# Kernel tuning notes

Measured on AMD Instinct MI355X. Metric: run time of the kernel, lower is better.

## Reference

```python
import jax, jax.numpy as jnp
import numpy as np

K = 5            # dimW
PARAM_SIGMA = 0.08
LAMBDA_V = 2.0
C_MID = 192


def _conv5(x, w, b):
    # standard 5x5 SAME conv (the linear 'm' term of INRF)
    y = jax.lax.conv_general_dilated(x, w, (1, 1), 'SAME',
                                     dimension_numbers=('NCHW', 'OIHW', 'NCHW'))
    return y + b[None, :, None, None]


def _inrf(x, m_w, m_b, w_w):
    """INRF layer: out = (m * x) - lambda * sum_y w(y) sigma(x(y) - (g*x)(center)).
    dimG=1 so the Gaussian g*x is the identity (center pixel). The radiometric
    nonlinearity sigma is a saturating tanh with slope 1/paramSigma.
    """
    B, C, H, W = x.shape
    # windowed gather: [B, C*K*K, H, W], channel-major / spatial-minor ordering
    patches = jax.lax.conv_general_dilated_patches(x, (K, K), (1, 1), 'SAME')
    patches = patches.reshape(B, C, K * K, H, W)
    s = jnp.tanh((patches - x[:, :, None]) / PARAM_SIGMA)   # [B,C,KK,H,W]
    wterm = jnp.einsum('bckhw,ock->bohw', s, w_w)           # [B,Cout,H,W]
    return _conv5(x, m_w, m_b) - LAMBDA_V * wterm


def _maxpool2(x):
    return jax.lax.reduce_window(x, -jnp.inf, jax.lax.max,
                                 (1, 1, 2, 2), (1, 1, 2, 2), 'VALID')


def _avgpool8(x):
    s = jax.lax.reduce_window(x, 0.0, jax.lax.add,
                              (1, 1, 8, 8), (1, 1, 8, 8), 'VALID')
    return s / 64.0


def setup_inputs() -> dict:
    key = jax.random.key(0)
    ks = jax.random.split(key, 11)
    B = 64
    f32 = jnp.float32
    return {
        'x':    jax.random.normal(ks[0], (B, 3, 32, 32), f32),
        'm1_w': jax.random.normal(ks[1], (C_MID, 3, K, K), f32) * 0.05,
        'm1_b': jnp.zeros((C_MID,), f32),
        'w1_w': jax.random.normal(ks[2], (C_MID, 3, K * K), f32) * 0.05,
        'm2_w': jax.random.normal(ks[3], (C_MID, C_MID, K, K), f32) * 0.02,
        'm2_b': jnp.zeros((C_MID,), f32),
        'w2_w': jax.random.normal(ks[4], (C_MID, C_MID, K * K), f32) * 0.02,
        'm3_w': jax.random.normal(ks[5], (C_MID, C_MID, K, K), f32) * 0.02,
        'm3_b': jnp.zeros((C_MID,), f32),
        'w3_w': jax.random.normal(ks[6], (C_MID, C_MID, K * K), f32) * 0.02,
        'fc_w': jax.random.normal(ks[7], (10, C_MID), f32) * 0.05,
        'fc_b': jnp.zeros((10,), f32),
    }


def reference(x, m1_w, m1_b, w1_w, m2_w, m2_b, w2_w,
              m3_w, m3_b, w3_w, fc_w, fc_b):
    # dropout layers run in eval mode (identity); dp2d1 has p=0.0 anyway
    x00 = _maxpool2(_inrf(x, m1_w, m1_b, w1_w))      # [B,192,16,16]
    x01 = _inrf(x00, m2_w, m2_b, w2_w)               # [B,192,16,16]
    x03 = _maxpool2(x01)                             # [B,192,8,8]
    x04 = _inrf(x03, m3_w, m3_b, w3_w)               # [B,192,8,8]
    x05 = _avgpool8(x04)                             # [B,192,1,1]
    feat = x05.reshape(-1, C_MID)
    logits = feat @ fc_w.T + fc_b                    # [B,10]
    return (logits, x00, x01)
```

## Files before the change

### kernel.cpp

```cpp
#include <hip/hip_runtime.h>
#include <math.h>

#define COUT 192
#define NF 12

typedef __bf16 bf16_8 __attribute__((ext_vector_type(8)));
typedef float  f32x4  __attribute__((ext_vector_type(4)));

__device__ __forceinline__ float fast_tanh125(float d) {
    float e = __builtin_amdgcn_exp2f(d * 36.06737602222409f);
    return 1.0f - 2.0f * __builtin_amdgcn_rcpf(e + 1.0f);
}

__device__ __forceinline__ void gl_lds16(const void* gptr, void* lptr) {
    auto g = (const __attribute__((address_space(1))) unsigned int*)gptr;
    auto l = (__attribute__((address_space(3))) unsigned int*)lptr;
    __builtin_amdgcn_global_load_lds(g, l, 16, 0, 0);
}

template<int CIN>
__global__ void prep_w(const float* __restrict__ m_w, const float* __restrict__ w_w,
                       __bf16* __restrict__ Bp) {
    int idx = blockIdx.x * 256 + threadIdx.x;
    const int total = CIN * 2 * NF * 64;
    if (idx >= total) return;
    int lane = idx & 63;
    int nf = (idx >> 6) % NF;
    int cc = idx / (NF * 64);
    int t = cc & 1, c = cc >> 1;
    int n = nf * 16 + (lane & 15);
    int k0 = (lane >> 4) * 8;
    bf16_8 v;
    #pragma unroll
    for (int e = 0; e < 8; ++e) {
        int k = k0 + e;
        float val = 0.f;
        if (k < 25) {
            val = (t == 0) ? m_w[((size_t)n * CIN + c) * 25 + k]
                           : -2.0f * w_w[((size_t)n * CIN + c) * 25 + k];
        }
        v[e] = (__bf16)val;
    }
    *(bf16_8*)(Bp + (size_t)idx * 8) = v;
}

__global__ __launch_bounds__(256, 3) void inrf1_mfma(
    const float* __restrict__ x, const __bf16* __restrict__ Bp,
    const float* __restrict__ bias, float* __restrict__ x00)
{
    __shared__ float win[3][6][36];
    __shared__ float hp[192][33];

    const int b  = blockIdx.x >> 4;
    const int h0 = (blockIdx.x & 15) * 2;
    const int tid = threadIdx.x;
    const int wv = tid >> 6, lane = tid & 63;
    const int hl = wv >> 1, half = wv & 1;
    const int mcol = lane & 15, q = lane >> 4;
    const int wpos = half * 16 + mcol;

    for (int i = tid; i < 3 * 6 * 36; i += 256) {
        int c = i / 216, r = (i / 36) % 6, cc = i % 36;
        int gr = h0 + r - 2, gc = cc - 2;
        float v = 0.f;
        if (gr >= 0 && gr < 32 && gc >= 0 && gc < 32)
            v = x[((size_t)(b * 3 + c) * 32 + gr) * 32 + gc];
        win[c][r][cc] = v;
    }
    __syncthreads();

    int offs[8];
    #pragma unroll
    for (int e = 0; e < 8; ++e) {
        int k = q * 8 + e;
        int kk = (k < 25) ? k : 0;
        offs[e] = (hl + kk / 5) * 36 + wpos + (kk % 5);
    }
    const int cen_off = (hl + 2) * 36 + wpos + 2;

    f32x4 acc[NF];
    #pragma unroll
    for (int j = 0; j < NF; ++j) acc[j] = (f32x4){0.f, 0.f, 0.f, 0.f};

    const float* winf = &win[0][0][0];
    for (int c = 0; c < 3; ++c) {
        const float* wf = winf + c * 216;
        float cen = wf[cen_off];
        bf16_8 av, as_;
        #pragma unroll
        for (int e = 0; e < 8; ++e) {
            float v = wf[offs[e]];
            av[e] = (__bf16)v;
            as_[e] = (__bf16)fast_tanh125(v - cen);
        }
        const bf16_8* b0 = (const bf16_8*)Bp + ((size_t)(c * 2 + 0) * NF) * 64 + lane;
        const bf16_8* b1 = b0 + NF * 64;
        #pragma unroll
        for (int j = 0; j < NF; ++j)
            acc[j] = __builtin_amdgcn_mfma_f32_16x16x32_bf16(av, b0[j * 64], acc[j], 0, 0, 0);
        #pragma unroll
        for (int j = 0; j < NF; ++j)
            acc[j] = __builtin_amdgcn_mfma_f32_16x16x32_bf16(as_, b1[j * 64], acc[j], 0, 0, 0);
    }

    #pragma unroll
    for (int j = 0; j < NF; ++j) {
        int n = j * 16 + mcol;
        hp[n][hl * 16 + half * 8 + q * 2 + 0] = fmaxf(acc[j][0], acc[j][1]);
        hp[n][hl * 16 + half * 8 + q * 2 + 1] = fmaxf(acc[j][2], acc[j][3]);
    }
    __syncthreads();

    const int hpout = h0 >> 1;
    for (int i = tid; i < 192 * 16; i += 256) {
        int n = i >> 4, wp = i & 15;
        float v = fmaxf(hp[n][wp], hp[n][16 + wp]) + bias[n];
        x00[((size_t)(b * COUT + n) * 16 + hpout) * 16 + wp] = v;
    }
}

__global__ __launch_bounds__(256, 1) void inrf2_mfma(
    const float* __restrict__ xin, const __bf16* __restrict__ Bp,
    float* __restrict__ out0, float* __restrict__ part)
{
    constexpr int CPS = 48;
    __shared__ __align__(16) __bf16 Bs[3][24 * 64 * 8];
    __shared__ float win[3][420];

    const int b  = blockIdx.x >> 2;
    const int ks = blockIdx.x & 3;
    const int c0 = ks * CPS;
    const int tid = threadIdx.x;
    const int wv = tid >> 6, lane = tid & 63;
    const int wp = lane & 15, q = lane >> 4;

    int offs[8];
    #pragma unroll
    for (int e = 0; e < 8; ++e) {
        int k = q * 8 + e;
        int kk = (k < 25) ? k : 0;
        offs[e] = (kk / 5) * 21 + (kk % 5);
    }

    const int j0 = tid, j1 = tid + 256;
    const int r0_ = j0 / 20, c0_ = j0 % 20;
    const int r1_ = j1 / 20, c1_ = j1 % 20;
    const int w0i = r0_ * 21 + c0_;
    const int w1i = r1_ * 21 + c1_;
    const bool in1 = j1 < 400;
    const bool ok0 = (r0_ >= 2 && r0_ < 18 && c0_ >= 2 && c0_ < 18);
    const bool ok1 = in1 && (r1_ >= 2 && r1_ < 18 && c1_ >= 2 && c1_ < 18);
    const float* xb = xin + (size_t)b * COUT * 256;

    f32x4 acc[4][12];
    #pragma unroll
    for (int m = 0; m < 4; ++m)
        #pragma unroll
        for (int j = 0; j < 12; ++j) acc[m][j] = (f32x4){0.f, 0.f, 0.f, 0.f};

#define BUILD_A(SLOT, AV, AS)                                              \
    {                                                                      \
        const float* wc = win[(SLOT)];                                     \
        _Pragma("unroll")                                                  \
        for (int m = 0; m < 4; ++m) {                                      \
            const int base = (wv * 4 + m) * 21 + wp;                       \
            float cen = wc[base + 44];                                     \
            _Pragma("unroll")                                              \
            for (int e = 0; e < 8; ++e) {                                  \
                float v = wc[base + offs[e]];                              \
                (AV)[m][e] = (__bf16)v;                                    \
                (AS)[m][e] = (__bf16)fast_tanh125(v - cen);                \
            }                                                              \
        }                                                                  \
    }

    #pragma unroll
    for (int rr = 0; rr < 2; ++rr) {
        const int c = c0 + rr;
        float v0 = 0.f, v1 = 0.f;
        if (ok0) v0 = xb[(size_t)c * 256 + (r0_ - 2) * 16 + (c0_ - 2)];
        if (ok1) v1 = xb[(size_t)c * 256 + (r1_ - 2) * 16 + (c1_ - 2)];
        const __bf16* gB = Bp + (size_t)c * 2 * NF * 64 * 8 + wv * 3072 + lane * 8;
        #pragma unroll
        for (int i = 0; i < 6; ++i)
            gl_lds16(gB + i * 512, &Bs[rr][wv * 3072 + i * 512]);
        win[rr][w0i] = v0;
        if (in1) win[rr][w1i] = v1;
    }
    __syncthreads();

    bf16_8 av[4], as_[4];
    BUILD_A(0, av, as_);

    #pragma unroll 3
    for (int r = 0; r < CPS; ++r) {
        const int sl_cur = r % 3;
        const int sl_n1  = (r + 1) % 3;
        const int sl_n2  = (r + 2) % 3;
        const bool do2 = (r + 2) < CPS;
        const bool do1 = (r + 1) < CPS;

        float v0 = 0.f, v1 = 0.f;
        if (do2) {
            const int c = c0 + r + 2;
            if (ok0) v0 = xb[(size_t)c * 256 + (r0_ - 2) * 16 + (c0_ - 2)];
            if (ok1) v1 = xb[(size_t)c * 256 + (r1_ - 2) * 16 + (c1_ - 2)];
            const __bf16* gB = Bp + (size_t)c * 2 * NF * 64 * 8 + wv * 3072 + lane * 8;
            #pragma unroll
            for (int i = 0; i < 6; ++i)
                gl_lds16(gB + i * 512, &Bs[sl_n2][wv * 3072 + i * 512]);
        }

        bf16_8 avN[4], asN[4];
        if (do1) BUILD_A(sl_n1, avN, asN);

        const bf16_8* Bf = (const bf16_8*)(Bs[sl_cur]) + lane;
        #pragma unroll
        for (int j = 0; j < 12; ++j) {
            bf16_8 fm = Bf[j * 64];
            bf16_8 fs = Bf[(12 + j) * 64];
            #pragma unroll
            for (int m = 0; m < 4; ++m) {
                acc[m][j] = __builtin_amdgcn_mfma_f32_16x16x32_bf16(av[m],  fm, acc[m][j], 0, 0, 0);
                acc[m][j] = __builtin_amdgcn_mfma_f32_16x16x32_bf16(as_[m], fs, acc[m][j], 0, 0, 0);
            }
        }

        if (do2) {
            win[sl_n2][w0i] = v0;
            if (in1) win[sl_n2][w1i] = v1;
        }

        if (do1) {
            #pragma unroll
            for (int m = 0; m < 4; ++m) { av[m] = avN[m]; as_[m] = asN[m]; }
        }
        __syncthreads();
    }
#undef BUILD_A

    float* outp = (ks == 0) ? out0 : (part + (size_t)(ks - 1) * 3145728);
    #pragma unroll
    for (int j = 0; j < 12; ++j) {
        int n = j * 16 + wp;
        #pragma unroll
        for (int m = 0; m < 4; ++m) {
            int h = wv * 4 + m;
            *(f32x4*)&outp[((size_t)(b * COUT + n)) * 256 + h * 16 + q * 4] = acc[m][j];
        }
    }
}

__global__ __launch_bounds__(512) void finish2(
    float* __restrict__ x01, const float* __restrict__ part,
    const float* __restrict__ bias, __bf16* __restrict__ An)
{
    __shared__ float xbuf[8][256];
    const int b  = blockIdx.x / 24;
    const int cg = blockIdx.x % 24;
    const int tid = threadIdx.x;
    const int wv = tid >> 6, lane = tid & 63;
    const int ch = cg * 8 + wv;

    float* p0 = x01 + ((size_t)b * COUT + ch) * 256;
    const float* pp = part + ((size_t)b * COUT + ch) * 256;
    const float bv = bias[ch];
    #pragma unroll
    for (int i = 0; i < 4; ++i) {
        int idx = lane + 64 * i;
        float s = ((p0[idx] + pp[idx]) + pp[idx + 3145728]) + pp[idx + 2 * 3145728] + bv;
        xbuf[wv][idx] = s;
        p0[idx] = s;
    }
    __syncthreads();

    const int ph = lane >> 3, pw = lane & 7;
    const int i0 = ph * 32 + pw * 2;
    float x8 = fmaxf(fmaxf(xbuf[wv][i0], xbuf[wv][i0 + 1]),
                     fmaxf(xbuf[wv][i0 + 16], xbuf[wv][i0 + 17]));

    float myT = 0.f, myW = 0.f;
    #pragma unroll
    for (int k = 0; k < 25; ++k) {
        const int dy = k / 5 - 2, dx = k % 5 - 2;
        const bool valid = (ph + dy >= 0) && (ph + dy < 8) && (pw + dx >= 0) && (pw + dx < 8);
        float nb = __shfl(x8, (lane + dy * 8 + dx) & 63);
        nb = valid ? nb : 0.f;
        float tS = fast_tanh125(nb - x8);
        float wS = nb;
        #pragma unroll
        for (int off = 1; off < 64; off <<= 1) {
            tS += __shfl_xor(tS, off);
            wS += __shfl_xor(wS, off);
        }
        if (lane == k) { myT = tS; myW = wS; }
    }

    const int mt = b >> 4;
    if (lane < 25) {
        const int k = lane;
        const int la = (k >> 3) * 16 + (b & 15);
        const int e = k & 7;
        const int ccW = ch * 2, ccT = ch * 2 + 1;
        An[((size_t)(ccW * 4 + mt) * 64 + la) * 8 + e] = (__bf16)(myW * 0.015625f);
        An[((size_t)(ccT * 4 + mt) * 64 + la) * 8 + e] = (__bf16)(myT * 0.015625f);
    } else if (lane < 32) {
        const int la = 3 * 16 + (b & 15);
        const int e = lane & 7;
        const int ccW = ch * 2, ccT = ch * 2 + 1;
        An[((size_t)(ccW * 4 + mt) * 64 + la) * 8 + e] = (__bf16)0.f;
        An[((size_t)(ccT * 4 + mt) * 64 + la) * 8 + e] = (__bf16)0.f;
    }
}

__global__ __launch_bounds__(512) void gemm3p(
    const __bf16* __restrict__ An, const __bf16* __restrict__ Bp,
    float* __restrict__ part)
{
    const int ks = blockIdx.x;
    const int tid = threadIdx.x;
    const int wv = tid >> 6, lane = tid & 63;
    const int mt = wv & 3, nh = wv >> 2;

    f32x4 acc[6];
    #pragma unroll
    for (int j = 0; j < 6; ++j) acc[j] = (f32x4){0.f, 0.f, 0.f, 0.f};

    for (int i = 0; i < 4; ++i) {
        const int cc = ks * 4 + i;
        bf16_8 a = *(const bf16_8*)(An + ((size_t)(cc * 4 + mt) * 64 + lane) * 8);
        #pragma unroll
        for (int j = 0; j < 6; ++j) {
            bf16_8 bw = *(const bf16_8*)(Bp + ((size_t)(cc * NF + nh * 6 + j) * 64 + lane) * 8);
            acc[j] = __builtin_amdgcn_mfma_f32_16x16x32_bf16(a, bw, acc[j], 0, 0, 0);
        }
    }
    #pragma unroll
    for (int j = 0; j < 6; ++j) {
        int n = (nh * 6 + j) * 16 + (lane & 15);
        *(f32x4*)(part + ((size_t)ks * COUT + n) * 64 + mt * 16 + (lane >> 4) * 4) = acc[j];
    }
}

__global__ __launch_bounds__(256) void logitsk(
    const float* __restrict__ part, const float* __restrict__ m3_b,
    const float* __restrict__ fc_w, const float* __restrict__ fc_b,
    float* __restrict__ logits)
{
    __shared__ float feat[COUT];
    const int b = blockIdx.x;
    const int t = threadIdx.x;
    if (t < COUT) {
        float s = 0.f;
        for (int ks = 0; ks < 96; ++ks) s += part[((size_t)ks * COUT + t) * 64 + b];
        feat[t] = s + m3_b[t];
    }
    __syncthreads();
    if (t < 10) {
        float s = fc_b[t];
        #pragma unroll 8
        for (int c = 0; c < COUT; ++c) s = fmaf(fc_w[t * COUT + c], feat[c], s);
        logits[(size_t)b * 10 + t] = s;
    }
}

extern "C" void kernel_launch(void* const* d_in, const int* in_sizes, int n_in,
                              void* d_out, int out_size, void* d_ws, size_t ws_size,
                              hipStream_t stream) {
    const float* x    = (const float*)d_in[0];
    const float* m1_w = (const float*)d_in[1];
    const float* m1_b = (const float*)d_in[2];
    const float* w1_w = (const float*)d_in[3];
    const float* m2_w = (const float*)d_in[4];
    const float* m2_b = (const float*)d_in[5];
    const float* w2_w = (const float*)d_in[6];
    const float* m3_w = (const float*)d_in[7];
    const float* m3_b = (const float*)d_in[8];
    const float* w3_w = (const float*)d_in[9];
    const float* fc_w = (const float*)d_in[10];
    const float* fc_b = (const float*)d_in[11];

    float* out = (float*)d_out;
    float* ws  = (float*)d_ws;

    float* logits = out;
    float* x00 = out + 640;
    float* x01 = out + 640 + 3145728;

    __bf16* Bp1  = (__bf16*)(ws);
    __bf16* Bp2  = (__bf16*)(ws + 18432);
    __bf16* Bp3  = (__bf16*)(ws + 1198080);
    __bf16* An   = (__bf16*)(ws + 2377728);
    float*  part2 = ws + 2770944;
    float*  part3 = ws + 2770944;

    prep_w<3>  <<<(3   * 2 * NF * 64 + 255) / 256, 256, 0, stream>>>(m1_w, w1_w, Bp1);
    prep_w<192><<<(192 * 2 * NF * 64 + 255) / 256, 256, 0, stream>>>(m2_w, w2_w, Bp2);
    prep_w<192><<<(192 * 2 * NF * 64 + 255) / 256, 256, 0, stream>>>(m3_w, w3_w, Bp3);

    inrf1_mfma<<<64 * 16, 256, 0, stream>>>(x, Bp1, m1_b, x00);
    inrf2_mfma<<<64 * 4, 256, 0, stream>>>(x00, Bp2, x01, part2);
    finish2<<<64 * 24, 512, 0, stream>>>(x01, part2, m2_b, An);
    gemm3p<<<96, 512, 0, stream>>>(An, Bp3, part3);
    logitsk<<<64, 256, 0, stream>>>(part3, m3_b, fc_w, fc_b, logits);
}
```

Before: 222.5 us.

## Split inrf2 output channels across two wave groups and merge weight-prep launches

The layer-2 INRF MFMA kernel now runs 512 threads per block, with eight waves instead of four. Each group of four waves covers the same 16 rows but only half of the 192 output channels, so accumulators per wave drop from 48 to 24 fragments and more waves are in flight. The A-fragment tanh/bf16 build is now duplicated across the two channel halves. The three weight-prep launches are combined into a single kernel to cut launch overhead.

Result: no change. 223.8 us (+0.6%).

```diff
diff --git a/kernel.cpp b/kernel.cpp
--- a/kernel.cpp
+++ b/kernel.cpp
@@ -18,15 +18,21 @@
     __builtin_amdgcn_global_load_lds(g, l, 16, 0, 0);
 }
 
-template<int CIN>
-__global__ void prep_w(const float* __restrict__ m_w, const float* __restrict__ w_w,
-                       __bf16* __restrict__ Bp) {
+__global__ void prep_all(const float* __restrict__ m1_w, const float* __restrict__ w1_w,
+                         const float* __restrict__ m2_w, const float* __restrict__ w2_w,
+                         const float* __restrict__ m3_w, const float* __restrict__ w3_w,
+                         __bf16* __restrict__ Bp1, __bf16* __restrict__ Bp2,
+                         __bf16* __restrict__ Bp3) {
     int idx = blockIdx.x * 256 + threadIdx.x;
-    const int total = CIN * 2 * NF * 64;
-    if (idx >= total) return;
-    int lane = idx & 63;
-    int nf = (idx >> 6) % NF;
-    int cc = idx / (NF * 64);
+    const int N1 = 3 * 2 * NF * 64, N2 = 192 * 2 * NF * 64;
+    const float *mw, *ww; __bf16* Bp; int CIN, li;
+    if (idx < N1)           { mw = m1_w; ww = w1_w; Bp = Bp1; CIN = 3;   li = idx; }
+    else if (idx < N1 + N2) { mw = m2_w; ww = w2_w; Bp = Bp2; CIN = 192; li = idx - N1; }
+    else if (idx < N1 + 2 * N2) { mw = m3_w; ww = w3_w; Bp = Bp3; CIN = 192; li = idx - N1 - N2; }
+    else return;
+    int lane = li & 63;
+    int nf = (li >> 6) % NF;
+    int cc = li / (NF * 64);
     int t = cc & 1, c = cc >> 1;
     int n = nf * 16 + (lane & 15);
     int k0 = (lane >> 4) * 8;
@@ -36,12 +42,12 @@
         int k = k0 + e;
         float val = 0.f;
         if (k < 25) {
-            val = (t == 0) ? m_w[((size_t)n * CIN + c) * 25 + k]
-                           : -2.0f * w_w[((size_t)n * CIN + c) * 25 + k];
+            val = (t == 0) ? mw[((size_t)n * CIN + c) * 25 + k]
+                           : -2.0f * ww[((size_t)n * CIN + c) * 25 + k];
         }
         v[e] = (__bf16)val;
     }
-    *(bf16_8*)(Bp + (size_t)idx * 8) = v;
+    *(bf16_8*)(Bp + (size_t)li * 8) = v;
 }
 
 __global__ __launch_bounds__(256, 3) void inrf1_mfma(
@@ -119,7 +125,7 @@
     }
 }
 
-__global__ __launch_bounds__(256, 1) void inrf2_mfma(
+__global__ __launch_bounds__(512, 2) void inrf2_mfma(
     const float* __restrict__ xin, const __bf16* __restrict__ Bp,
     float* __restrict__ out0, float* __restrict__ part)
 {
@@ -132,6 +138,7 @@
     const int c0 = ks * CPS;
     const int tid = threadIdx.x;
     const int wv = tid >> 6, lane = tid & 63;
+    const int mg = wv & 3, nh = wv >> 2;
     const int wp = lane & 15, q = lane >> 4;
 
     int offs[8];
@@ -142,28 +149,24 @@
         offs[e] = (kk / 5) * 21 + (kk % 5);
     }
 
-    const int j0 = tid, j1 = tid + 256;
-    const int r0_ = j0 / 20, c0_ = j0 % 20;
-    const int r1_ = j1 / 20, c1_ = j1 % 20;
+    const int r0_ = tid / 20, c0_ = tid % 20;
     const int w0i = r0_ * 21 + c0_;
-    const int w1i = r1_ * 21 + c1_;
-    const bool in1 = j1 < 400;
-    const bool ok0 = (r0_ >= 2 && r0_ < 18 && c0_ >= 2 && c0_ < 18);
-    const bool ok1 = in1 && (r1_ >= 2 && r1_ < 18 && c1_ >= 2 && c1_ < 18);
+    const bool in0 = tid < 400;
+    const bool ok0 = in0 && (r0_ >= 2 && r0_ < 18 && c0_ >= 2 && c0_ < 18);
     const float* xb = xin + (size_t)b * COUT * 256;
 
-    f32x4 acc[4][12];
+    f32x4 acc[4][6];
     #pragma unroll
     for (int m = 0; m < 4; ++m)
         #pragma unroll
-        for (int j = 0; j < 12; ++j) acc[m][j] = (f32x4){0.f, 0.f, 0.f, 0.f};
+        for (int j = 0; j < 6; ++j) acc[m][j] = (f32x4){0.f, 0.f, 0.f, 0.f};
 
 #define BUILD_A(SLOT, AV, AS)                                              \
     {                                                                      \
         const float* wc = win[(SLOT)];                                     \
         _Pragma("unroll")                                                  \
         for (int m = 0; m < 4; ++m) {                                      \
-            const int base = (wv * 4 + m) * 21 + wp;                       \
+            const int base = (mg * 4 + m) * 21 + wp;                       \
             float cen = wc[base + 44];                                     \
             _Pragma("unroll")                                              \
             for (int e = 0; e < 8; ++e) {                                  \
@@ -177,15 +180,13 @@
     #pragma unroll
     for (int rr = 0; rr < 2; ++rr) {
         const int c = c0 + rr;
-        float v0 = 0.f, v1 = 0.f;
+        float v0 = 0.f;
         if (ok0) v0 = xb[(size_t)c * 256 + (r0_ - 2) * 16 + (c0_ - 2)];
-        if (ok1) v1 = xb[(size_t)c * 256 + (r1_ - 2) * 16 + (c1_ - 2)];
-        const __bf16* gB = Bp + (size_t)c * 2 * NF * 64 * 8 + wv * 3072 + lane * 8;
-        #pragma unroll
-        for (int i = 0; i < 6; ++i)
-            gl_lds16(gB + i * 512, &Bs[rr][wv * 3072 + i * 512]);
-        win[rr][w0i] = v0;
-        if (in1) win[rr][w1i] = v1;
+        const __bf16* gB = Bp + (size_t)c * 12288 + wv * 1536 + lane * 8;
+        #pragma unroll
+        for (int i = 0; i < 3; ++i)
+            gl_lds16(gB + i * 512, &Bs[rr][wv * 1536 + i * 512]);
+        if (in0) win[rr][w0i] = v0;
     }
     __syncthreads();
 
@@ -200,15 +201,14 @@
         const bool do2 = (r + 2) < CPS;
         const bool do1 = (r + 1) < CPS;
 
-        float v0 = 0.f, v1 = 0.f;
+        float v0 = 0.f;
         if (do2) {
             const int c = c0 + r + 2;
             if (ok0) v0 = xb[(size_t)c * 256 + (r0_ - 2) * 16 + (c0_ - 2)];
-            if (ok1) v1 = xb[(size_t)c * 256 + (r1_ - 2) * 16 + (c1_ - 2)];
-            const __bf16* gB = Bp + (size_t)c * 2 * NF * 64 * 8 + wv * 3072 + lane * 8;
+            const __bf16* gB = Bp + (size_t)c * 12288 + wv * 1536 + lane * 8;
             #pragma unroll
-            for (int i = 0; i < 6; ++i)
-                gl_lds16(gB + i * 512, &Bs[sl_n2][wv * 3072 + i * 512]);
+            for (int i = 0; i < 3; ++i)
+                gl_lds16(gB + i * 512, &Bs[sl_n2][wv * 1536 + i * 512]);
         }
 
         bf16_8 avN[4], asN[4];
@@ -216,9 +216,9 @@
 
         const bf16_8* Bf = (const bf16_8*)(Bs[sl_cur]) + lane;
         #pragma unroll
-        for (int j = 0; j < 12; ++j) {
-            bf16_8 fm = Bf[j * 64];
-            bf16_8 fs = Bf[(12 + j) * 64];
+        for (int j = 0; j < 6; ++j) {
+            bf16_8 fm = Bf[(nh * 6 + j) * 64];
+            bf16_8 fs = Bf[(12 + nh * 6 + j) * 64];
             #pragma unroll
             for (int m = 0; m < 4; ++m) {
                 acc[m][j] = __builtin_amdgcn_mfma_f32_16x16x32_bf16(av[m],  fm, acc[m][j], 0, 0, 0);
@@ -226,10 +226,7 @@
             }
         }
 
-        if (do2) {
-            win[sl_n2][w0i] = v0;
-            if (in1) win[sl_n2][w1i] = v1;
-        }
+        if (do2 && in0) win[sl_n2][w0i] = v0;
 
         if (do1) {
             #pragma unroll
@@ -241,11 +238,11 @@
 
     float* outp = (ks == 0) ? out0 : (part + (size_t)(ks - 1) * 3145728);
     #pragma unroll
-    for (int j = 0; j < 12; ++j) {
-        int n = j * 16 + wp;
+    for (int j = 0; j < 6; ++j) {
+        int n = (nh * 6 + j) * 16 + wp;
         #pragma unroll
         for (int m = 0; m < 4; ++m) {
-            int h = wv * 4 + m;
+            int h = mg * 4 + m;
             *(f32x4*)&outp[((size_t)(b * COUT + n)) * 256 + h * 16 + q * 4] = acc[m][j];
         }
     }
@@ -394,12 +391,10 @@
     float*  part2 = ws + 2770944;
     float*  part3 = ws + 2770944;
 
-    prep_w<3>  <<<(3   * 2 * NF * 64 + 255) / 256, 256, 0, stream>>>(m1_w, w1_w, Bp1);
-    prep_w<192><<<(192 * 2 * NF * 64 + 255) / 256, 256, 0, stream>>>(m2_w, w2_w, Bp2);
-    prep_w<192><<<(192 * 2 * NF * 64 + 255) / 256, 256, 0, stream>>>(m3_w, w3_w, Bp3);
+    prep_all<<<2322, 256, 0, stream>>>(m1_w, w1_w, m2_w, w2_w, m3_w, w3_w, Bp1, Bp2, Bp3);
 
     inrf1_mfma<<<64 * 16, 256, 0, stream>>>(x, Bp1, m1_b, x00);
-    inrf2_mfma<<<64 * 4, 256, 0, stream>>>(x00, Bp2, x01, part2);
+    inrf2_mfma<<<64 * 4, 512, 0, stream>>>(x00, Bp2, x01, part2);
     finish2<<<64 * 24, 512, 0, stream>>>(x01, part2, m2_b, An);
     gemm3p<<<96, 512, 0, stream>>>(An, Bp3, part3);
     logitsk<<<64, 256, 0, stream>>>(part3, m3_b, fc_w, fc_b, logits);
```
